# Optimization experiments

Measured on AMD Instinct MI355X. Metric: run time of the kernel, lower is better.

The kernel has to match this reference:

```python
import jax, jax.numpy as jnp
import numpy as np

CROP_H = 14
CROP_W = 14
EXTRAPOLATION_VALUE = 0.0


def setup_inputs() -> dict:
    key = jax.random.key(0)
    k1, k2, k3 = jax.random.split(key, 3)
    image = jax.random.normal(k1, (8, 256, 100, 100), dtype=jnp.float32)
    boxes = jax.random.uniform(k2, (512, 4), dtype=jnp.float32)  # (y1,x1,y2,x2) normalized
    box_ind = jax.random.randint(k3, (512,), 0, 8, dtype=jnp.int32)
    return {"image": image, "boxes": boxes, "box_ind": box_ind}


def _crop_and_resize(image, boxes, box_ind):
    # TF crop_and_resize semantics (bilinear), image in NCHW like the torch port.
    B, C, H, W = image.shape
    N = boxes.shape[0]
    y1, x1, y2, x2 = boxes[:, 0], boxes[:, 1], boxes[:, 2], boxes[:, 3]

    hs = jnp.arange(CROP_H, dtype=image.dtype)
    ws = jnp.arange(CROP_W, dtype=image.dtype)

    if CROP_H > 1:
        in_y = y1[:, None] * (H - 1) + hs[None, :] * ((y2 - y1) * (H - 1) / (CROP_H - 1))[:, None]
    else:
        in_y = (0.5 * (y1 + y2) * (H - 1))[:, None] * jnp.ones((1, CROP_H), image.dtype)
    if CROP_W > 1:
        in_x = x1[:, None] * (W - 1) + ws[None, :] * ((x2 - x1) * (W - 1) / (CROP_W - 1))[:, None]
    else:
        in_x = (0.5 * (x1 + x2) * (W - 1))[:, None] * jnp.ones((1, CROP_W), image.dtype)

    valid_y = (in_y >= 0) & (in_y <= H - 1)          # [N, ch]
    valid_x = (in_x >= 0) & (in_x <= W - 1)          # [N, cw]
    valid = valid_y[:, :, None] & valid_x[:, None, :]  # [N, ch, cw]

    yc = jnp.clip(in_y, 0.0, H - 1)
    xc = jnp.clip(in_x, 0.0, W - 1)
    y0 = jnp.floor(yc)
    x0 = jnp.floor(xc)
    ly = yc - y0  # y lerp weight [N, ch]
    lx = xc - x0  # x lerp weight [N, cw]
    y0i = y0.astype(jnp.int32)
    x0i = x0.astype(jnp.int32)
    y1i = jnp.minimum(y0i + 1, H - 1)
    x1i = jnp.minimum(x0i + 1, W - 1)

    b = box_ind[:, None, None]  # [N,1,1]

    def gather(yi, xi):
        # advanced indices (b, yi, xi) broadcast to [N, ch, cw]; channel slice -> [N, ch, cw, C]
        return image[b, :, yi[:, :, None], xi[:, None, :]]

    tl = gather(y0i, x0i)
    tr = gather(y0i, x1i)
    bl = gather(y1i, x0i)
    br = gather(y1i, x1i)

    lx_ = lx[:, None, :, None]
    ly_ = ly[:, :, None, None]
    top = tl + (tr - tl) * lx_
    bot = bl + (br - bl) * lx_
    val = top + (bot - top) * ly_  # [N, ch, cw, C]

    val = jnp.where(valid[..., None], val, jnp.asarray(EXTRAPOLATION_VALUE, image.dtype))
    return jnp.transpose(val, (0, 3, 1, 2))  # [N, C, ch, cw]


def reference(image, boxes, box_ind):
    return _crop_and_resize(image, boxes, box_ind)
```

## Files before the change

kernel.cpp:

```cpp
#include <hip/hip_runtime.h>
#include <hip/hip_fp16.h>

#define CROP_H 14
#define CROP_W 14
#define CROP_HW 196
#define CROP_HWP 98
#define CROP_HWQ 49
#define IMG_H 100
#define IMG_W 100
#define PLANE 10000
#define NCH 256
#define NBOX 512
#define NIMG 8

#define GEO_BYTES ((size_t)NBOX * CROP_HW * 8)
#define WS_NEED   GEO_BYTES

__global__ __launch_bounds__(256) void geom_kernel(
    const float* __restrict__ boxes, const int* __restrict__ box_ind,
    uint2* __restrict__ geo)
{
    __shared__ int s_lt[8], s_eq[8];

    const int n    = blockIdx.x;
    const int t    = threadIdx.x;
    const int lane = t & 63;
    const int wv   = t >> 6;
    const int bn   = box_ind[n];

    #pragma unroll
    for (int r = 0; r < 2; ++r) {
        const int m  = r * 256 + t;
        const int bm = box_ind[m];
        const unsigned long long lt = __ballot(bm < bn);
        const unsigned long long eq = __ballot(bm == bn);
        const int rel = n - (r * 256 + wv * 64);
        const unsigned long long pre =
            (rel <= 0) ? 0ull : ((rel >= 64) ? ~0ull : ((1ull << rel) - 1ull));
        if (lane == 0) {
            s_lt[wv * 2 + r] = __popcll(lt);
            s_eq[wv * 2 + r] = __popcll(eq & pre);
        }
    }
    __syncthreads();
    int slot = 0;
    #pragma unroll
    for (int i = 0; i < 8; ++i) slot += s_lt[i] + s_eq[i];

    if (t >= CROP_HW) return;
    const int h = t / CROP_W;
    const int w = t - h * CROP_W;

    const float4 bx = reinterpret_cast<const float4*>(boxes)[n];
    const float y1 = bx.x, x1 = bx.y, y2 = bx.z, x2 = bx.w;

    const float scale_y = (y2 - y1) * (float)(IMG_H - 1) / (float)(CROP_H - 1);
    const float scale_x = (x2 - x1) * (float)(IMG_W - 1) / (float)(CROP_W - 1);

    const float in_y = y1 * (float)(IMG_H - 1) + (float)h * scale_y;
    const float in_x = x1 * (float)(IMG_W - 1) + (float)w * scale_x;

    const bool valid = (in_y >= 0.0f) & (in_y <= (float)(IMG_H - 1)) &
                       (in_x >= 0.0f) & (in_x <= (float)(IMG_W - 1));

    const float yc = fminf(fmaxf(in_y, 0.0f), (float)(IMG_H - 1));
    const float xc = fminf(fmaxf(in_x, 0.0f), (float)(IMG_W - 1));

    const float y0f = floorf(yc);
    const float x0f = floorf(xc);
    const float ly = yc - y0f;
    const float lx = xc - x0f;

    const int y0  = (int)y0f;
    const int x0  = (int)x0f;
    const int dy  = min(y0 + 1, IMG_H - 1) - y0;

    const unsigned pk = (unsigned)(y0 * IMG_W + x0)
                      | ((unsigned)dy << 15)
                      | (valid ? (1u << 16) : 0u) | ((unsigned)n << 17);

    const __half2 hh = __floats2half2_rn(lx, ly);
    const unsigned hbits = *reinterpret_cast<const unsigned*>(&hh);

    geo[slot * CROP_HW + t] = make_uint2(pk, hbits);
}

__device__ __forceinline__ float bilerp_h2(const __half2* __restrict__ sp,
                                           unsigned pk, unsigned hbits)
{
    const int o   = (int)(pk & 0x3FFFu);
    const int dyo = (int)((pk >> 15) & 1u) * IMG_W;
    const __half2 h = *reinterpret_cast<const __half2*>(&hbits);
    const float lx = __low2float(h);
    const float ly = __high2float(h);
    const float wm = (pk & (1u << 16)) ? 1.0f : 0.0f;

    const __half2 tp = sp[o];
    const __half2 bp = sp[o + dyo];

    const float tl = __low2float(tp), tr = __high2float(tp);
    const float bl = __low2float(bp), br = __high2float(bp);

    const float top = tl + (tr - tl) * lx;
    const float bot = bl + (br - bl) * lx;
    return (top + (bot - top) * ly) * wm;
}

__global__ __launch_bounds__(512, 4) void crop_resize_main(
    const float* __restrict__ image,
    const int*   __restrict__ box_ind,
    const uint2* __restrict__ geo,
    float* __restrict__ out)
{
    __shared__ __half2 s_pairs[PLANE];
    __shared__ int s_ltm[8], s_eqm[8];

    const int blk = blockIdx.x;
    const int b   = blk >> 8;
    const int c   = blk & 255;
    const int t   = threadIdx.x;
    const int lane = t & 63;
    const int wv   = t >> 6;

    {
        const int bm = box_ind[t];
        const unsigned long long lt = __ballot(bm < b);
        const unsigned long long eq = __ballot(bm == b);
        if (lane == 0) { s_ltm[wv] = __popcll(lt); s_eqm[wv] = __popcll(eq); }
    }

    const float* __restrict__ plane =
        image + ((size_t)(b * NCH + c)) * PLANE;
    const float4* __restrict__ plane_g = reinterpret_cast<const float4*>(plane);

    for (int i = t; i < PLANE / 4; i += 512) {
        const float4 f = plane_g[i];
        const int m    = i % (IMG_W / 4);
        const int base = 4 * i;
        const float nx = plane[base + ((m == (IMG_W / 4 - 1)) ? 3 : 4)];
        s_pairs[base + 0] = __floats2half2_rn(f.x, f.y);
        s_pairs[base + 1] = __floats2half2_rn(f.y, f.z);
        s_pairs[base + 2] = __floats2half2_rn(f.z, f.w);
        s_pairs[base + 3] = __floats2half2_rn(f.w, nx);
    }
    __syncthreads();

    int sb = 0, nb = 0;
    #pragma unroll
    for (int i = 0; i < 8; ++i) { sb += s_ltm[i]; nb += s_eqm[i]; }

    const int totalq = nb * CROP_HWQ;
    if (totalq == 0) return;

    const uint4* __restrict__ geo4 =
        reinterpret_cast<const uint4*>(geo) + (size_t)sb * CROP_HWP;
    float* __restrict__ outc = out + (size_t)c * CROP_HW;

    int q = t;
    while (q >= totalq) q -= totalq;
    uint4 ga = geo4[2 * q];
    uint4 gb = geo4[2 * q + 1];

    const int iters = (totalq + 511) >> 9;
    for (int it = 0; it < iters; ++it) {
        int qn = q + 512;
        while (qn >= totalq) qn -= totalq;
        const uint4 gna = geo4[2 * qn];
        const uint4 gnb = geo4[2 * qn + 1];

        const unsigned n = ga.x >> 17;
        const int j = q - (q / CROP_HWQ) * CROP_HWQ;

        float4 val;
        val.x = bilerp_h2(s_pairs, ga.x, ga.y);
        val.y = bilerp_h2(s_pairs, ga.z, ga.w);
        val.z = bilerp_h2(s_pairs, gb.x, gb.y);
        val.w = bilerp_h2(s_pairs, gb.z, gb.w);

        *reinterpret_cast<float4*>(outc + (size_t)n * (NCH * CROP_HW) + j * 4) = val;

        q = qn; ga = gna; gb = gnb;
    }
}

__global__ __launch_bounds__(256) void crop_resize_simple(
    const float* __restrict__ image, const float* __restrict__ boxes,
    const int* __restrict__ box_ind, float* __restrict__ out)
{
    const int n = blockIdx.y;
    const int i = blockIdx.x * 256 + threadIdx.x;
    const int c  = i / CROP_HW;
    const int hw = i - c * CROP_HW;
    const int h  = hw / CROP_W;
    const int w  = hw - h * CROP_W;

    const float y1 = boxes[n * 4 + 0];
    const float x1 = boxes[n * 4 + 1];
    const float y2 = boxes[n * 4 + 2];
    const float x2 = boxes[n * 4 + 3];
    const int   b  = box_ind[n];

    const float scale_y = (y2 - y1) * (float)(IMG_H - 1) / (float)(CROP_H - 1);
    const float scale_x = (x2 - x1) * (float)(IMG_W - 1) / (float)(CROP_W - 1);
    const float in_y = y1 * (float)(IMG_H - 1) + (float)h * scale_y;
    const float in_x = x1 * (float)(IMG_W - 1) + (float)w * scale_x;
    const bool valid = (in_y >= 0.0f) & (in_y <= (float)(IMG_H - 1)) &
                       (in_x >= 0.0f) & (in_x <= (float)(IMG_W - 1));
    const float yc = fminf(fmaxf(in_y, 0.0f), (float)(IMG_H - 1));
    const float xc = fminf(fmaxf(in_x, 0.0f), (float)(IMG_W - 1));
    const float y0f = floorf(yc), x0f = floorf(xc);
    const float ly = yc - y0f, lx = xc - x0f;
    const int y0 = (int)y0f, x0 = (int)x0f;
    const int y1i = min(y0 + 1, IMG_H - 1), x1i = min(x0 + 1, IMG_W - 1);

    const float* __restrict__ p = image + ((size_t)(b * NCH + c)) * PLANE;
    const float tl = p[y0  * IMG_W + x0];
    const float tr = p[y0  * IMG_W + x1i];
    const float bl = p[y1i * IMG_W + x0];
    const float br = p[y1i * IMG_W + x1i];
    const float top = tl + (tr - tl) * lx;
    const float bot = bl + (br - bl) * lx;
    float val = top + (bot - top) * ly;
    out[(size_t)n * (NCH * CROP_HW) + i] = valid ? val : 0.0f;
}

extern "C" void kernel_launch(void* const* d_in, const int* in_sizes, int n_in,
                              void* d_out, int out_size, void* d_ws, size_t ws_size,
                              hipStream_t stream) {
    const float* image   = (const float*)d_in[0];
    const float* boxes   = (const float*)d_in[1];
    const int*   box_ind = (const int*)d_in[2];
    float* out = (float*)d_out;

    if (ws_size < WS_NEED) {
        dim3 grid(196, NBOX);
        crop_resize_simple<<<grid, dim3(256), 0, stream>>>(image, boxes, box_ind, out);
        return;
    }

    uint2* geo = (uint2*)d_ws;

    geom_kernel<<<dim3(NBOX), dim3(256), 0, stream>>>(boxes, box_ind, geo);
    crop_resize_main<<<dim3(NIMG * NCH), dim3(512), 0, stream>>>(image, box_ind, geo, out);
}
```

Measured before the change: 44.45 us.

## Prefetch all geometry records before staging plane into LDS

Box-slot counting now uses per-wave ballots over all 512 boxes instead of a shared-memory reduction, so each thread knows its work range before the barrier. Up to eight iterations of geometry records are then loaded into registers before the image plane is converted into LDS, overlapping the geo fetch latency with the plane staging. This removes the serial load-compute chain of the old software-pipelined loop. The cost is much higher register pressure (16 uint4 per thread) at launch bounds 512,4, which may cause spills or lower occupancy, and the code path is duplicated.

```diff
diff --git a/kernel.cpp b/kernel.cpp
--- a/kernel.cpp
+++ b/kernel.cpp
@@ -12,6 +12,7 @@
 #define NCH 256
 #define NBOX 512
 #define NIMG 8
+#define MAXI 8
 
 #define GEO_BYTES ((size_t)NBOX * CROP_HW * 8)
 #define WS_NEED   GEO_BYTES
@@ -113,73 +114,111 @@
     float* __restrict__ out)
 {
     __shared__ __half2 s_pairs[PLANE];
-    __shared__ int s_ltm[8], s_eqm[8];
 
     const int blk = blockIdx.x;
     const int b   = blk >> 8;
     const int c   = blk & 255;
     const int t   = threadIdx.x;
     const int lane = t & 63;
-    const int wv   = t >> 6;
-
-    {
-        const int bm = box_ind[t];
-        const unsigned long long lt = __ballot(bm < b);
-        const unsigned long long eq = __ballot(bm == b);
-        if (lane == 0) { s_ltm[wv] = __popcll(lt); s_eqm[wv] = __popcll(eq); }
-    }
+
+    int sb = 0, nb = 0;
+    #pragma unroll
+    for (int r = 0; r < 8; ++r) {
+        const int bm = box_ind[r * 64 + lane];
+        sb += __popcll(__ballot(bm < b));
+        nb += __popcll(__ballot(bm == b));
+    }
+
+    const int totalq = nb * CROP_HWQ;
+    const int iters  = (totalq + 511) >> 9;
+    const uint4* __restrict__ geo4 =
+        reinterpret_cast<const uint4*>(geo) + (size_t)sb * CROP_HWP;
 
     const float* __restrict__ plane =
         image + ((size_t)(b * NCH + c)) * PLANE;
     const float4* __restrict__ plane_g = reinterpret_cast<const float4*>(plane);
-
-    for (int i = t; i < PLANE / 4; i += 512) {
-        const float4 f = plane_g[i];
-        const int m    = i % (IMG_W / 4);
-        const int base = 4 * i;
-        const float nx = plane[base + ((m == (IMG_W / 4 - 1)) ? 3 : 4)];
-        s_pairs[base + 0] = __floats2half2_rn(f.x, f.y);
-        s_pairs[base + 1] = __floats2half2_rn(f.y, f.z);
-        s_pairs[base + 2] = __floats2half2_rn(f.z, f.w);
-        s_pairs[base + 3] = __floats2half2_rn(f.w, nx);
-    }
-    __syncthreads();
-
-    int sb = 0, nb = 0;
-    #pragma unroll
-    for (int i = 0; i < 8; ++i) { sb += s_ltm[i]; nb += s_eqm[i]; }
-
-    const int totalq = nb * CROP_HWQ;
-    if (totalq == 0) return;
-
-    const uint4* __restrict__ geo4 =
-        reinterpret_cast<const uint4*>(geo) + (size_t)sb * CROP_HWP;
     float* __restrict__ outc = out + (size_t)c * CROP_HW;
 
-    int q = t;
-    while (q >= totalq) q -= totalq;
-    uint4 ga = geo4[2 * q];
-    uint4 gb = geo4[2 * q + 1];
-
-    const int iters = (totalq + 511) >> 9;
-    for (int it = 0; it < iters; ++it) {
-        int qn = q + 512;
-        while (qn >= totalq) qn -= totalq;
-        const uint4 gna = geo4[2 * qn];
-        const uint4 gnb = geo4[2 * qn + 1];
-
-        const unsigned n = ga.x >> 17;
-        const int j = q - (q / CROP_HWQ) * CROP_HWQ;
-
-        float4 val;
-        val.x = bilerp_h2(s_pairs, ga.x, ga.y);
-        val.y = bilerp_h2(s_pairs, ga.z, ga.w);
-        val.z = bilerp_h2(s_pairs, gb.x, gb.y);
-        val.w = bilerp_h2(s_pairs, gb.z, gb.w);
-
-        *reinterpret_cast<float4*>(outc + (size_t)n * (NCH * CROP_HW) + j * 4) = val;
-
-        q = qn; ga = gna; gb = gnb;
+    if (totalq >= 512) {
+        int  q[MAXI + 1];
+        uint4 ga[MAXI], gb[MAXI];
+        q[0] = t;
+        #pragma unroll
+        for (int i = 0; i < MAXI; ++i) {
+            const uint4* gp = geo4 + 2 * (size_t)q[i];
+            ga[i] = gp[0];
+            gb[i] = gp[1];
+            const int qn = q[i] + 512;
+            q[i + 1] = (qn >= totalq) ? qn - totalq : qn;
+        }
+
+        for (int i = t; i < PLANE / 4; i += 512) {
+            const float4 f = plane_g[i];
+            const int m    = i % (IMG_W / 4);
+            const int base = 4 * i;
+            const float nx = plane[base + ((m == (IMG_W / 4 - 1)) ? 3 : 4)];
+            s_pairs[base + 0] = __floats2half2_rn(f.x, f.y);
+            s_pairs[base + 1] = __floats2half2_rn(f.y, f.z);
+            s_pairs[base + 2] = __floats2half2_rn(f.z, f.w);
+            s_pairs[base + 3] = __floats2half2_rn(f.w, nx);
+        }
+        __syncthreads();
+
+        #pragma unroll
+        for (int i = 0; i < MAXI; ++i) {
+            if (i < iters) {
+                const unsigned n = ga[i].x >> 17;
+                const int j = q[i] - (q[i] / CROP_HWQ) * CROP_HWQ;
+                float4 val;
+                val.x = bilerp_h2(s_pairs, ga[i].x, ga[i].y);
+                val.y = bilerp_h2(s_pairs, ga[i].z, ga[i].w);
+                val.z = bilerp_h2(s_pairs, gb[i].x, gb[i].y);
+                val.w = bilerp_h2(s_pairs, gb[i].z, gb[i].w);
+                *reinterpret_cast<float4*>(
+                    outc + (size_t)n * (NCH * CROP_HW) + j * 4) = val;
+            }
+        }
+        int qc = q[MAXI];
+        for (int it = MAXI; it < iters; ++it) {
+            const uint4 a = geo4[2 * qc];
+            const uint4 bq = geo4[2 * qc + 1];
+            const unsigned n = a.x >> 17;
+            const int j = qc - (qc / CROP_HWQ) * CROP_HWQ;
+            float4 val;
+            val.x = bilerp_h2(s_pairs, a.x, a.y);
+            val.y = bilerp_h2(s_pairs, a.z, a.w);
+            val.z = bilerp_h2(s_pairs, bq.x, bq.y);
+            val.w = bilerp_h2(s_pairs, bq.z, bq.w);
+            *reinterpret_cast<float4*>(
+                outc + (size_t)n * (NCH * CROP_HW) + j * 4) = val;
+            const int qn = qc + 512;
+            qc = (qn >= totalq) ? qn - totalq : qn;
+        }
+    } else {
+        for (int i = t; i < PLANE / 4; i += 512) {
+            const float4 f = plane_g[i];
+            const int m    = i % (IMG_W / 4);
+            const int base = 4 * i;
+            const float nx = plane[base + ((m == (IMG_W / 4 - 1)) ? 3 : 4)];
+            s_pairs[base + 0] = __floats2half2_rn(f.x, f.y);
+            s_pairs[base + 1] = __floats2half2_rn(f.y, f.z);
+            s_pairs[base + 2] = __floats2half2_rn(f.z, f.w);
+            s_pairs[base + 3] = __floats2half2_rn(f.w, nx);
+        }
+        __syncthreads();
+        for (int qc = t; qc < totalq; qc += 512) {
+            const uint4 a = geo4[2 * qc];
+            const uint4 bq = geo4[2 * qc + 1];
+            const unsigned n = a.x >> 17;
+            const int j = qc - (qc / CROP_HWQ) * CROP_HWQ;
+            float4 val;
+            val.x = bilerp_h2(s_pairs, a.x, a.y);
+            val.y = bilerp_h2(s_pairs, a.z, a.w);
+            val.z = bilerp_h2(s_pairs, bq.x, bq.y);
+            val.w = bilerp_h2(s_pairs, bq.z, bq.w);
+            *reinterpret_cast<float4*>(
+                outc + (size_t)n * (NCH * CROP_HW) + j * 4) = val;
+        }
     }
 }
 
```

Measured after the change: 46.54 us. +4.7%, slower.

## Process two channels per block with channel-interleaved half2 shared plane

Applied to the files above, without the earlier changes.

Each block now loads two adjacent channel planes and packs them as half2 pairs (channel0, channel1) per pixel in shared memory, instead of packing horizontal neighbour pairs for one channel. Every geometry entry is then reused for two output channels, which halves the geometry reads and block count and amortises the box-index counting per block. The cost is four LDS reads per sample instead of two, plus an extra dx bit in the packed geometry. The box_ind scan also moves from a shared-memory reduction to per-wave ballots over all 512 entries.

```diff
diff --git a/kernel.cpp b/kernel.cpp
--- a/kernel.cpp
+++ b/kernel.cpp
@@ -74,9 +74,10 @@
     const int y0  = (int)y0f;
     const int x0  = (int)x0f;
     const int dy  = min(y0 + 1, IMG_H - 1) - y0;
+    const int dx  = min(x0 + 1, IMG_W - 1) - x0;
 
     const unsigned pk = (unsigned)(y0 * IMG_W + x0)
-                      | ((unsigned)dy << 15)
+                      | ((unsigned)dx << 14) | ((unsigned)dy << 15)
                       | (valid ? (1u << 16) : 0u) | ((unsigned)n << 17);
 
     const __half2 hh = __floats2half2_rn(lx, ly);
@@ -85,25 +86,36 @@
     geo[slot * CROP_HW + t] = make_uint2(pk, hbits);
 }
 
-__device__ __forceinline__ float bilerp_h2(const __half2* __restrict__ sp,
-                                           unsigned pk, unsigned hbits)
+__device__ __forceinline__ float2 bilerp_du(const __half2* __restrict__ sp,
+                                            unsigned pk, unsigned hbits)
 {
     const int o   = (int)(pk & 0x3FFFu);
+    const int dx  = (int)((pk >> 14) & 1u);
     const int dyo = (int)((pk >> 15) & 1u) * IMG_W;
     const __half2 h = *reinterpret_cast<const __half2*>(&hbits);
     const float lx = __low2float(h);
     const float ly = __high2float(h);
     const float wm = (pk & (1u << 16)) ? 1.0f : 0.0f;
 
-    const __half2 tp = sp[o];
-    const __half2 bp = sp[o + dyo];
-
-    const float tl = __low2float(tp), tr = __high2float(tp);
-    const float bl = __low2float(bp), br = __high2float(bp);
-
-    const float top = tl + (tr - tl) * lx;
-    const float bot = bl + (br - bl) * lx;
-    return (top + (bot - top) * ly) * wm;
+    const __half2 tl2 = sp[o];
+    const __half2 tr2 = sp[o + dx];
+    const __half2 bl2 = sp[o + dyo];
+    const __half2 br2 = sp[o + dyo + dx];
+
+    const float tl0 = __low2float(tl2),  tl1 = __high2float(tl2);
+    const float tr0 = __low2float(tr2),  tr1 = __high2float(tr2);
+    const float bl0 = __low2float(bl2),  bl1 = __high2float(bl2);
+    const float br0 = __low2float(br2),  br1 = __high2float(br2);
+
+    const float top0 = tl0 + (tr0 - tl0) * lx;
+    const float bot0 = bl0 + (br0 - bl0) * lx;
+    const float top1 = tl1 + (tr1 - tl1) * lx;
+    const float bot1 = bl1 + (br1 - bl1) * lx;
+
+    float2 r;
+    r.x = (top0 + (bot0 - top0) * ly) * wm;
+    r.y = (top1 + (bot1 - top1) * ly) * wm;
+    return r;
 }
 
 __global__ __launch_bounds__(512, 4) void crop_resize_main(
@@ -112,49 +124,44 @@
     const uint2* __restrict__ geo,
     float* __restrict__ out)
 {
-    __shared__ __half2 s_pairs[PLANE];
-    __shared__ int s_ltm[8], s_eqm[8];
+    __shared__ __half2 s_du[PLANE];
 
     const int blk = blockIdx.x;
-    const int b   = blk >> 8;
-    const int c   = blk & 255;
+    const int b   = blk >> 7;
+    const int cp  = blk & 127;
+    const int c0  = cp * 2;
     const int t   = threadIdx.x;
     const int lane = t & 63;
-    const int wv   = t >> 6;
-
-    {
-        const int bm = box_ind[t];
-        const unsigned long long lt = __ballot(bm < b);
-        const unsigned long long eq = __ballot(bm == b);
-        if (lane == 0) { s_ltm[wv] = __popcll(lt); s_eqm[wv] = __popcll(eq); }
-    }
-
-    const float* __restrict__ plane =
-        image + ((size_t)(b * NCH + c)) * PLANE;
-    const float4* __restrict__ plane_g = reinterpret_cast<const float4*>(plane);
-
-    for (int i = t; i < PLANE / 4; i += 512) {
-        const float4 f = plane_g[i];
-        const int m    = i % (IMG_W / 4);
-        const int base = 4 * i;
-        const float nx = plane[base + ((m == (IMG_W / 4 - 1)) ? 3 : 4)];
-        s_pairs[base + 0] = __floats2half2_rn(f.x, f.y);
-        s_pairs[base + 1] = __floats2half2_rn(f.y, f.z);
-        s_pairs[base + 2] = __floats2half2_rn(f.z, f.w);
-        s_pairs[base + 3] = __floats2half2_rn(f.w, nx);
-    }
-    __syncthreads();
 
     int sb = 0, nb = 0;
     #pragma unroll
-    for (int i = 0; i < 8; ++i) { sb += s_ltm[i]; nb += s_eqm[i]; }
+    for (int r = 0; r < 8; ++r) {
+        const int bm = box_ind[r * 64 + lane];
+        sb += __popcll(__ballot(bm < b));
+        nb += __popcll(__ballot(bm == b));
+    }
+
+    const float* __restrict__ p0 = image + ((size_t)(b * NCH + c0)) * PLANE;
+    const float4* __restrict__ p0g = reinterpret_cast<const float4*>(p0);
+    const float4* __restrict__ p1g = reinterpret_cast<const float4*>(p0 + PLANE);
+
+    for (int i = t; i < PLANE / 4; i += 512) {
+        const float4 f0 = p0g[i];
+        const float4 f1 = p1g[i];
+        const int base = 4 * i;
+        s_du[base + 0] = __floats2half2_rn(f0.x, f1.x);
+        s_du[base + 1] = __floats2half2_rn(f0.y, f1.y);
+        s_du[base + 2] = __floats2half2_rn(f0.z, f1.z);
+        s_du[base + 3] = __floats2half2_rn(f0.w, f1.w);
+    }
+    __syncthreads();
 
     const int totalq = nb * CROP_HWQ;
     if (totalq == 0) return;
 
     const uint4* __restrict__ geo4 =
         reinterpret_cast<const uint4*>(geo) + (size_t)sb * CROP_HWP;
-    float* __restrict__ outc = out + (size_t)c * CROP_HW;
+    float* __restrict__ outc = out + (size_t)c0 * CROP_HW;
 
     int q = t;
     while (q >= totalq) q -= totalq;
@@ -171,13 +178,14 @@
         const unsigned n = ga.x >> 17;
         const int j = q - (q / CROP_HWQ) * CROP_HWQ;
 
-        float4 val;
-        val.x = bilerp_h2(s_pairs, ga.x, ga.y);
-        val.y = bilerp_h2(s_pairs, ga.z, ga.w);
-        val.z = bilerp_h2(s_pairs, gb.x, gb.y);
-        val.w = bilerp_h2(s_pairs, gb.z, gb.w);
-
-        *reinterpret_cast<float4*>(outc + (size_t)n * (NCH * CROP_HW) + j * 4) = val;
+        const float2 r0 = bilerp_du(s_du, ga.x, ga.y);
+        const float2 r1 = bilerp_du(s_du, ga.z, ga.w);
+        const float2 r2 = bilerp_du(s_du, gb.x, gb.y);
+        const float2 r3 = bilerp_du(s_du, gb.z, gb.w);
+
+        float* dst = outc + (size_t)n * (NCH * CROP_HW) + j * 4;
+        *reinterpret_cast<float4*>(dst) = make_float4(r0.x, r1.x, r2.x, r3.x);
+        *reinterpret_cast<float4*>(dst + CROP_HW) = make_float4(r0.y, r1.y, r2.y, r3.y);
 
         q = qn; ga = gna; gb = gnb;
     }
@@ -241,5 +249,5 @@
     uint2* geo = (uint2*)d_ws;
 
     geom_kernel<<<dim3(NBOX), dim3(256), 0, stream>>>(boxes, box_ind, geo);
-    crop_resize_main<<<dim3(NIMG * NCH), dim3(512), 0, stream>>>(image, box_ind, geo, out);
-}
+    crop_resize_main<<<dim3(NIMG * (NCH / 2)), dim3(512), 0, stream>>>(image, box_ind, geo, out);
+}
```

Measured after the change: 40.02 us. 10.0% less time.
